# Performance work log

Measured on AMD Instinct MI355X. Metric: run time of the kernel, lower is better.

## Reference

```python
import jax, jax.numpy as jnp
import numpy as np

EPS = 1e-5

def _conv1x1(x, w):
    # x: (B, Cin, N, K), w: (Cout, Cin) -> (B, Cout, N, K)
    return jnp.einsum('oc,bcnk->bonk', w, x)

def _bn2d(x, gamma, beta):
    # eval-mode BN with running_mean=0, running_var=1 (fresh init)
    scale = gamma / jnp.sqrt(1.0 + EPS)
    return x * scale[None, :, None, None] + beta[None, :, None, None]

def setup_inputs() -> dict:
    key = jax.random.key(0)
    ks = jax.random.split(key, 10)
    B, Cin, N, K = 8, 64, 1024, 32
    Cout, M = 64, 8
    Cin2 = 2 * Cin  # kernel_input='w_neighbor'
    features = jax.random.normal(ks[0], (B, Cin, N, K), dtype=jnp.float32)
    points_xyz = jax.random.normal(ks[1], (B, 3, N, K), dtype=jnp.float32)
    # ScoreNet convs: mlp_channels [7,16,16,16,M]; first 3 have BN (no bias), last has bias
    w1 = jax.random.normal(ks[2], (16, 7), dtype=jnp.float32) * (2.0 / 7) ** 0.5
    w2 = jax.random.normal(ks[3], (16, 16), dtype=jnp.float32) * (2.0 / 16) ** 0.5
    w3 = jax.random.normal(ks[4], (16, 16), dtype=jnp.float32) * (2.0 / 16) ** 0.5
    w4 = jax.random.normal(ks[5], (M, 16), dtype=jnp.float32) * (2.0 / 16) ** 0.5
    b4 = jnp.zeros((M,), dtype=jnp.float32)
    g1 = jnp.ones((16,), jnp.float32); be1 = jnp.zeros((16,), jnp.float32)
    g2 = jnp.ones((16,), jnp.float32); be2 = jnp.zeros((16,), jnp.float32)
    g3 = jnp.ones((16,), jnp.float32); be3 = jnp.zeros((16,), jnp.float32)
    # weight bank: kaiming_normal on (M, 2Cin, Cout) -> stored as (2Cin, M, Cout)
    wb = jax.random.normal(ks[6], (Cin2, M, Cout), dtype=jnp.float32) * (2.0 / Cin2) ** 0.5
    bn_g = jnp.ones((Cout,), jnp.float32); bn_b = jnp.zeros((Cout,), jnp.float32)
    return dict(features=features, points_xyz=points_xyz,
                w1=w1, g1=g1, be1=be1, w2=w2, g2=g2, be2=be2,
                w3=w3, g3=g3, be3=be3, w4=w4, b4=b4,
                weight_bank=wb, bn_g=bn_g, bn_b=bn_b)

def reference(features, points_xyz, w1, g1, be1, w2, g2, be2, w3, g3, be3,
              w4, b4, weight_bank, bn_g, bn_b):
    B, Cin, N, K = features.shape
    M = weight_bank.shape[1]
    # kernel_input = 'w_neighbor': concat(feat - center, feat) -> (B, 2Cin, N, K)
    center_f = features[..., :1]
    feat = jnp.concatenate([features - center_f, features], axis=1)
    # scorenet input = 'w_neighbor_dist': (center_xyz, xyz_diff, dist) -> (B, 7, N, K)
    center_xyz = jnp.broadcast_to(points_xyz[..., :1], points_xyz.shape)
    xyz_diff = points_xyz - center_xyz
    dist = jnp.sqrt(jnp.sum(xyz_diff * xyz_diff, axis=1, keepdims=True))
    xyz_feats = jnp.concatenate([center_xyz, xyz_diff, dist], axis=1)
    h = jax.nn.relu(_bn2d(_conv1x1(xyz_feats, w1), g1, be1))
    h = jax.nn.relu(_bn2d(_conv1x1(h, w2), g2, be2))
    h = jax.nn.relu(_bn2d(_conv1x1(h, w3), g3, be3))
    s = _conv1x1(h, w4) + b4[None, :, None, None]  # (B, M, N, K)
    scores = jax.nn.softmax(s, axis=1)
    scores = jnp.transpose(scores, (0, 2, 3, 1))  # (B, N, K, M)
    # matmul with weight bank then score-weighted sum over kernels, fused via einsum
    # original: (B,N,K,2Cin)@(2Cin,M*Cout) -> (B,N,K,M,Cout); sum_m scores * . -> (B,N,K,Cout)
    new_features = jnp.einsum('bcnk,cmo,bnkm->bonk', feat, weight_bank, scores)
    # BN2d (eval, fresh stats) + ReLU
    new_features = jax.nn.relu(_bn2d(new_features, bn_g, bn_b))
    return new_features
```

## Files before the change

### kernel.cpp

```cpp
#include <hip/hip_runtime.h>
#include <hip/hip_bf16.h>

typedef _Float16 f16;
typedef __attribute__((ext_vector_type(2))) _Float16 f16x2;
typedef __attribute__((ext_vector_type(8))) _Float16 f16x8;
typedef __attribute__((ext_vector_type(16))) float f32x16;

#define BNSCL 0.9999950000375f

__global__ __launch_bounds__(256) void k_scores(
    const float* __restrict__ xyz,
    const float* __restrict__ w1, const float* __restrict__ g1, const float* __restrict__ be1,
    const float* __restrict__ w2, const float* __restrict__ g2, const float* __restrict__ be2,
    const float* __restrict__ w3, const float* __restrict__ g3, const float* __restrict__ be3,
    const float* __restrict__ w4, const float* __restrict__ b4,
    const float* __restrict__ wb, f16* __restrict__ wbtA,
    f16* __restrict__ scores)
{
    __shared__ float lw[856];
    const int tid = threadIdx.x;

    if (blockIdx.x < 256) {
        int idx = blockIdx.x * 256 + tid;
        int j    = idx & 7;
        int lane = (idx >> 3) & 63;
        int ks   = (idx >> 9) & 63;
        int ot   = idx >> 15;
        int cp   = ks * 2 + (lane >> 5);
        int o    = ot * 32 + (lane & 31);
        wbtA[idx] = (f16)wb[(cp * 8 + j) * 64 + o];
    }

    if (tid < 112) lw[tid] = w1[tid];
    lw[112 + tid] = w2[tid];
    lw[368 + tid] = w3[tid];
    if (tid < 128) lw[624 + tid] = w4[tid];
    if (tid < 8)   lw[752 + tid] = b4[tid];
    if (tid < 16) {
        lw[760 + tid] = g1[tid] * BNSCL;  lw[776 + tid] = be1[tid];
        lw[792 + tid] = g2[tid] * BNSCL;  lw[808 + tid] = be2[tid];
        lw[824 + tid] = g3[tid] * BNSCL;  lw[840 + tid] = be3[tid];
    }
    __syncthreads();

    float in7[2][7], h1[2][16], h2[2][16], s[2][8];

#pragma unroll
    for (int q = 0; q < 2; ++q) {
        int g = blockIdx.x * 512 + q * 256 + tid;
        int b = g >> 15;
        int p = g & 32767;
        int pc = p & ~31;
        const float* xb = xyz + (size_t)b * 98304;
        float cx = xb[pc], cy = xb[32768 + pc], cz = xb[65536 + pc];
        float dx = xb[p] - cx, dy = xb[32768 + p] - cy, dz = xb[65536 + p] - cz;
        in7[q][0] = cx; in7[q][1] = cy; in7[q][2] = cz;
        in7[q][3] = dx; in7[q][4] = dy; in7[q][5] = dz;
        in7[q][6] = sqrtf(dx * dx + dy * dy + dz * dz);
    }

#pragma unroll
    for (int o = 0; o < 16; ++o) {
        float a0 = 0.f, a1 = 0.f;
#pragma unroll
        for (int c = 0; c < 7; ++c) {
            float w = lw[o * 7 + c];
            a0 += w * in7[0][c]; a1 += w * in7[1][c];
        }
        float gs = lw[760 + o], bb = lw[776 + o];
        h1[0][o] = fmaxf(a0 * gs + bb, 0.f);
        h1[1][o] = fmaxf(a1 * gs + bb, 0.f);
    }
#pragma unroll
    for (int o = 0; o < 16; ++o) {
        float a0 = 0.f, a1 = 0.f;
#pragma unroll
        for (int c = 0; c < 16; ++c) {
            float w = lw[112 + o * 16 + c];
            a0 += w * h1[0][c]; a1 += w * h1[1][c];
        }
        float gs = lw[792 + o], bb = lw[808 + o];
        h2[0][o] = fmaxf(a0 * gs + bb, 0.f);
        h2[1][o] = fmaxf(a1 * gs + bb, 0.f);
    }
#pragma unroll
    for (int o = 0; o < 16; ++o) {
        float a0 = 0.f, a1 = 0.f;
#pragma unroll
        for (int c = 0; c < 16; ++c) {
            float w = lw[368 + o * 16 + c];
            a0 += w * h2[0][c]; a1 += w * h2[1][c];
        }
        float gs = lw[824 + o], bb = lw[840 + o];
        h1[0][o] = fmaxf(a0 * gs + bb, 0.f);
        h1[1][o] = fmaxf(a1 * gs + bb, 0.f);
    }
#pragma unroll
    for (int o = 0; o < 8; ++o) {
        float bb = lw[752 + o];
        float a0 = bb, a1 = bb;
#pragma unroll
        for (int c = 0; c < 16; ++c) {
            float w = lw[624 + o * 16 + c];
            a0 += w * h1[0][c]; a1 += w * h1[1][c];
        }
        s[0][o] = a0; s[1][o] = a1;
    }

#pragma unroll
    for (int q = 0; q < 2; ++q) {
        int g = blockIdx.x * 512 + q * 256 + tid;
        float mx = s[q][0];
#pragma unroll
        for (int i = 1; i < 8; ++i) mx = fmaxf(mx, s[q][i]);
        float sum = 0.f;
#pragma unroll
        for (int i = 0; i < 8; ++i) { s[q][i] = __expf(s[q][i] - mx); sum += s[q][i]; }
        float inv = 1.f / sum;
        f16x8 o8;
#pragma unroll
        for (int i = 0; i < 8; ++i) o8[i] = (f16)(s[q][i] * inv);
        *(f16x8*)(scores + (size_t)g * 8) = o8;
    }
}

__global__ __launch_bounds__(512, 4) void k_main(
    const float* __restrict__ feat,
    const f16* __restrict__ scores,
    const f16* __restrict__ wbtA,
    const float* __restrict__ bn_g, const float* __restrict__ bn_b,
    float* __restrict__ out)
{
    __shared__ __align__(16) f16 lwb[32768];

    const int tid  = threadIdx.x;
    const int lane = tid & 63;
    const int wave = tid >> 6;
    const int l31  = lane & 31;
    const int lh   = lane >> 5;

    const int ot = blockIdx.x >> 9;
    const int g  = blockIdx.x & 511;
    const int pblock = g * 512;
    const int b    = pblock >> 15;
    const int pt0  = (pblock & 32767) + wave * 64;
    const int pc0  = pt0 + l31;
    const int pc1  = pc0 + 32;

    const float* fb  = feat + (size_t)b * 2097152;
    const float* frb = fb + ((size_t)lh << 15);

    float pA[4], pB[4], pC[4], pD[4];
#pragma unroll
    for (int d = 0; d < 4; ++d) {
        const float* fr = frb + ((size_t)d << 16);
        pA[d] = fr[pc0]; pB[d] = fr[pc1]; pC[d] = fr[pt0]; pD[d] = fr[pt0 + 32];
    }

    const int gpt = pblock + wave * 64 + l31;
    f16x8 sv0 = *(const f16x8*)(scores + (size_t)gpt * 8);
    f16x8 sv1 = *(const f16x8*)(scores + (size_t)(gpt + 32) * 8);

    const f16* src = wbtA + ((size_t)ot << 15);
#pragma unroll
    for (int it = 0; it < 8; ++it) {
        int idx = it * 512 + tid;
        *(int4*)&lwb[idx << 3] = *(const int4*)&src[idx << 3];
    }
    __syncthreads();

    const f16x2 s0a = {sv0[0], sv0[1]}, s0b = {sv0[2], sv0[3]},
                s0c = {sv0[4], sv0[5]}, s0d = {sv0[6], sv0[7]};
    const f16x2 s1a = {sv1[0], sv1[1]}, s1b = {sv1[2], sv1[3]},
                s1c = {sv1[4], sv1[5]}, s1d = {sv1[6], sv1[7]};

    f32x16 acc0 = {}, acc1 = {};

    const f16* Alds = lwb + (lane << 3);

#define KSTEP(kk, RELOAD)                                                      \
    {                                                                          \
        const int d_ = (kk) & 3;                                               \
        float fv0 = pA[d_], fv1 = pB[d_], fc0 = pC[d_], fc1 = pD[d_];          \
        if (RELOAD) {                                                          \
            const float* fr_ = frb + ((size_t)((kk) + 4) << 16);               \
            pA[d_] = fr_[pc0]; pB[d_] = fr_[pc1];                              \
            pC[d_] = fr_[pt0]; pD[d_] = fr_[pt0 + 32];                         \
        }                                                                      \
        f16x8 aD = *(const f16x8*)(Alds + ((size_t)(kk) << 9));                \
        f16x8 aR = *(const f16x8*)(Alds + ((size_t)((kk) + 32) << 9));         \
        f16 hR0 = (f16)fv0,          hR1 = (f16)fv1;                           \
        f16 hD0 = (f16)(fv0 - fc0),  hD1 = (f16)(fv1 - fc1);                   \
        f16x2 fR0 = {hR0, hR0}, fR1 = {hR1, hR1};                              \
        f16x2 fD0 = {hD0, hD0}, fD1 = {hD1, hD1};                              \
        f16x2 d0a = fD0 * s0a, d0b = fD0 * s0b, d0c = fD0 * s0c, d0d = fD0 * s0d; \
        f16x2 d1a = fD1 * s1a, d1b = fD1 * s1b, d1c = fD1 * s1c, d1d = fD1 * s1d; \
        f16x2 r0a = fR0 * s0a, r0b = fR0 * s0b, r0c = fR0 * s0c, r0d = fR0 * s0d; \
        f16x2 r1a = fR1 * s1a, r1b = fR1 * s1b, r1c = fR1 * s1c, r1d = fR1 * s1d; \
        f16x8 bD0 = {d0a[0],d0a[1],d0b[0],d0b[1],d0c[0],d0c[1],d0d[0],d0d[1]}; \
        f16x8 bD1 = {d1a[0],d1a[1],d1b[0],d1b[1],d1c[0],d1c[1],d1d[0],d1d[1]}; \
        f16x8 bR0 = {r0a[0],r0a[1],r0b[0],r0b[1],r0c[0],r0c[1],r0d[0],r0d[1]}; \
        f16x8 bR1 = {r1a[0],r1a[1],r1b[0],r1b[1],r1c[0],r1c[1],r1d[0],r1d[1]}; \
        acc0 = __builtin_amdgcn_mfma_f32_32x32x16_f16(aD, bD0, acc0, 0, 0, 0); \
        acc1 = __builtin_amdgcn_mfma_f32_32x32x16_f16(aD, bD1, acc1, 0, 0, 0); \
        acc0 = __builtin_amdgcn_mfma_f32_32x32x16_f16(aR, bR0, acc0, 0, 0, 0); \
        acc1 = __builtin_amdgcn_mfma_f32_32x32x16_f16(aR, bR1, acc1, 0, 0, 0); \
    }

#define KS4(b0, R) KSTEP(b0, R) KSTEP((b0)+1, R) KSTEP((b0)+2, R) KSTEP((b0)+3, R)
    KS4(0, 1)  KS4(4, 1)  KS4(8, 1)  KS4(12, 1)
    KS4(16, 1) KS4(20, 1) KS4(24, 1) KS4(28, 0)
#undef KS4
#undef KSTEP

#pragma unroll
    for (int r = 0; r < 16; ++r) {
        int o = ot * 32 + (r & 3) + ((r >> 2) << 3) + (lh << 2);
        float gs = bn_g[o] * BNSCL, bb = bn_b[o];
        size_t row = (size_t)(b * 64 + o) << 15;
        out[row + pc0] = fmaxf(acc0[r] * gs + bb, 0.f);
        out[row + pc1] = fmaxf(acc1[r] * gs + bb, 0.f);
    }
}

extern "C" void kernel_launch(void* const* d_in, const int* in_sizes, int n_in,
                              void* d_out, int out_size, void* d_ws, size_t ws_size,
                              hipStream_t stream)
{
    const float* features = (const float*)d_in[0];
    const float* xyz      = (const float*)d_in[1];
    const float* w1  = (const float*)d_in[2];
    const float* g1  = (const float*)d_in[3];
    const float* be1 = (const float*)d_in[4];
    const float* w2  = (const float*)d_in[5];
    const float* g2  = (const float*)d_in[6];
    const float* be2 = (const float*)d_in[7];
    const float* w3  = (const float*)d_in[8];
    const float* g3  = (const float*)d_in[9];
    const float* be3 = (const float*)d_in[10];
    const float* w4  = (const float*)d_in[11];
    const float* b4  = (const float*)d_in[12];
    const float* wb  = (const float*)d_in[13];
    const float* bn_g = (const float*)d_in[14];
    const float* bn_b = (const float*)d_in[15];

    f16* scores = (f16*)d_ws;
    f16* wbtA   = (f16*)((char*)d_ws + (4u << 20));

    k_scores<<<512, 256, 0, stream>>>(xyz, w1, g1, be1, w2, g2, be2,
                                      w3, g3, be3, w4, b4, wb, wbtA, scores);
    k_main<<<1024, 512, 0, stream>>>(features, scores, wbtA, bn_g, bn_b,
                                     (float*)d_out);
}
```

Before: 182.0 us.

## Stream feature rows into LDS via async global_load_lds ring buffer

```diff
diff --git a/kernel.cpp b/kernel.cpp
--- a/kernel.cpp
+++ b/kernel.cpp
@@ -132,34 +132,25 @@
     float* __restrict__ out)
 {
     __shared__ __align__(16) f16 lwb[32768];
+    __shared__ __align__(16) float fbuf[4][2][512];
 
     const int tid  = threadIdx.x;
     const int lane = tid & 63;
     const int wave = tid >> 6;
     const int l31  = lane & 31;
     const int lh   = lane >> 5;
+    const int w64  = wave * 64;
 
     const int ot = blockIdx.x >> 9;
     const int g  = blockIdx.x & 511;
     const int pblock = g * 512;
     const int b    = pblock >> 15;
-    const int pt0  = (pblock & 32767) + wave * 64;
+    const int pt0  = (pblock & 32767) + w64;
     const int pc0  = pt0 + l31;
     const int pc1  = pc0 + 32;
 
-    const float* fb  = feat + (size_t)b * 2097152;
-    const float* frb = fb + ((size_t)lh << 15);
-
-    float pA[4], pB[4], pC[4], pD[4];
-#pragma unroll
-    for (int d = 0; d < 4; ++d) {
-        const float* fr = frb + ((size_t)d << 16);
-        pA[d] = fr[pc0]; pB[d] = fr[pc1]; pC[d] = fr[pt0]; pD[d] = fr[pt0 + 32];
-    }
-
-    const int gpt = pblock + wave * 64 + l31;
-    f16x8 sv0 = *(const f16x8*)(scores + (size_t)gpt * 8);
-    f16x8 sv1 = *(const f16x8*)(scores + (size_t)(gpt + 32) * 8);
+    const float* fb = feat + (size_t)b * 2097152;
+    const float* gsrc0 = fb + (pblock & 32767) + w64 + lane;
 
     const f16* src = wbtA + ((size_t)ot << 15);
 #pragma unroll
@@ -167,28 +158,49 @@
         int idx = it * 512 + tid;
         *(int4*)&lwb[idx << 3] = *(const int4*)&src[idx << 3];
     }
-    __syncthreads();
-
+
+    const int gpt = pblock + w64 + l31;
+    f16x8 sv0 = *(const f16x8*)(scores + (size_t)gpt * 8);
+    f16x8 sv1 = *(const f16x8*)(scores + (size_t)(gpt + 32) * 8);
     const f16x2 s0a = {sv0[0], sv0[1]}, s0b = {sv0[2], sv0[3]},
                 s0c = {sv0[4], sv0[5]}, s0d = {sv0[6], sv0[7]};
     const f16x2 s1a = {sv1[0], sv1[1]}, s1b = {sv1[2], sv1[3]},
                 s1c = {sv1[4], sv1[5]}, s1d = {sv1[6], sv1[7]};
 
     f32x16 acc0 = {}, acc1 = {};
-
     const f16* Alds = lwb + (lane << 3);
 
-#define KSTEP(kk, RELOAD)                                                      \
+#define STAGE(t)                                                               \
     {                                                                          \
-        const int d_ = (kk) & 3;                                               \
-        float fv0 = pA[d_], fv1 = pB[d_], fc0 = pC[d_], fc1 = pD[d_];          \
-        if (RELOAD) {                                                          \
-            const float* fr_ = frb + ((size_t)((kk) + 4) << 16);               \
-            pA[d_] = fr_[pc0]; pB[d_] = fr_[pc1];                              \
-            pC[d_] = fr_[pt0]; pD[d_] = fr_[pt0 + 32];                         \
-        }                                                                      \
+        __builtin_amdgcn_global_load_lds(                                      \
+            (const __attribute__((address_space(1))) void*)                    \
+                (gsrc0 + ((size_t)(2 * (t)) << 15)),                           \
+            (__attribute__((address_space(3))) void*)&fbuf[(t) & 3][0][w64],   \
+            4, 0, 0);                                                          \
+        __builtin_amdgcn_global_load_lds(                                      \
+            (const __attribute__((address_space(1))) void*)                    \
+                (gsrc0 + ((size_t)(2 * (t) + 1) << 15)),                       \
+            (__attribute__((address_space(3))) void*)&fbuf[(t) & 3][1][w64],   \
+            4, 0, 0);                                                          \
+    }
+
+#define WAITV(n) asm volatile("s_waitcnt vmcnt(" #n ")" ::: "memory")
+
+    __builtin_amdgcn_sched_barrier(0);
+    STAGE(0); STAGE(1); STAGE(2);
+
+    asm volatile("s_waitcnt lgkmcnt(0)" ::: "memory");
+    __builtin_amdgcn_s_barrier();
+
+#define KSTEP(kk, N)                                                           \
+    {                                                                          \
+        if ((kk) + 3 <= 31) { STAGE((kk) + 3); }                               \
+        WAITV(N);                                                              \
         f16x8 aD = *(const f16x8*)(Alds + ((size_t)(kk) << 9));                \
         f16x8 aR = *(const f16x8*)(Alds + ((size_t)((kk) + 32) << 9));         \
+        const float* frow = fbuf[(kk) & 3][lh];                                \
+        float fv0 = frow[w64 + l31], fv1 = frow[w64 + l31 + 32];               \
+        float fc0 = frow[w64],       fc1 = frow[w64 + 32];                     \
         f16 hR0 = (f16)fv0,          hR1 = (f16)fv1;                           \
         f16 hD0 = (f16)(fv0 - fc0),  hD1 = (f16)(fv1 - fc1);                   \
         f16x2 fR0 = {hR0, hR0}, fR1 = {hR1, hR1};                              \
@@ -207,11 +219,16 @@
         acc1 = __builtin_amdgcn_mfma_f32_32x32x16_f16(aR, bR1, acc1, 0, 0, 0); \
     }
 
-#define KS4(b0, R) KSTEP(b0, R) KSTEP((b0)+1, R) KSTEP((b0)+2, R) KSTEP((b0)+3, R)
-    KS4(0, 1)  KS4(4, 1)  KS4(8, 1)  KS4(12, 1)
-    KS4(16, 1) KS4(20, 1) KS4(24, 1) KS4(28, 0)
+#define KS4(b0) KSTEP(b0, 6) KSTEP((b0)+1, 6) KSTEP((b0)+2, 6) KSTEP((b0)+3, 6)
+    KS4(0)  KS4(4)  KS4(8)  KS4(12)
+    KS4(16) KS4(20) KS4(24)
+    KSTEP(28, 6) KSTEP(29, 4) KSTEP(30, 2) KSTEP(31, 0)
 #undef KS4
 #undef KSTEP
+#undef STAGE
+#undef WAITV
+
+    __builtin_amdgcn_sched_barrier(0);
 
 #pragma unroll
     for (int r = 0; r < 16; ++r) {
```

After: 174.9 us. 1.04x faster.
